# Kernel tuning notes

Hardware: AMD Instinct MI355X
Metric: run time of the kernel (lower is better)

Reference implementation:

```python
import jax, jax.numpy as jnp
import numpy as np

M = 12288   # anchor nodes
N = 12288   # neighbor nodes
D = 128     # out_features
TEMPERATURE = 0.07
NEG_PAD = jnp.float32(-2**32 + 1)  # same padding constant as torch code


def setup_inputs() -> dict:
    key = jax.random.key(0)
    k1, k2, k3, k4 = jax.random.split(key, 4)
    xx_anchor = jax.random.normal(k1, (M, D), dtype=jnp.float32)
    inp = jax.random.normal(k2, (N, D), dtype=jnp.float32)
    # sparse binary adjacency (~avg degree 25), stored dense int32 since the
    # module calls adj.to_dense() and only tests adj > 0
    adj = (jax.random.uniform(k3, (M, N)) < 0.002).astype(jnp.int32)
    # xavier_uniform-style init for the [D, D] attention weight
    limit = jnp.sqrt(6.0 / (D + D)).astype(jnp.float32)
    weight = jax.random.uniform(k4, (D, D), minval=-limit, maxval=limit, dtype=jnp.float32)
    return {"xx_anchor": xx_anchor, "input": inp, "adj": adj, "weight": weight}


def reference(xx_anchor, input, adj, weight):
    # scores[m, n] = (xx_anchor @ W) . input_n   -> dense [M, N]
    anchor_adj = jnp.einsum('md,de,ne->mn', xx_anchor, weight, input)
    scores = jnp.where(adj > 0, anchor_adj, NEG_PAD)
    atten = jax.nn.softmax(scores / TEMPERATURE, axis=1)  # row softmax over neighbors
    return atten @ input  # [M, D]
```

## Files before the change

### kernel.cpp

```cpp
#include <hip/hip_runtime.h>
#include <hip/hip_bf16.h>

#define M_ROWS 12288
#define N_COLS 12288
#define DDIM   128
#define MAXN   768
#define INV_T  (1.0f / 0.07f)

__global__ __launch_bounds__(256)
void layerconv_main(const float* __restrict__ xa,
                    const float* __restrict__ inp,
                    const int*   __restrict__ adj,
                    const float* __restrict__ wgt,
                    float*       __restrict__ out)
{
    const int m    = blockIdx.x;
    const int tid  = threadIdx.x;
    const int lane = tid & 63;
    const int wid  = tid >> 6;

    __shared__ float xarow[DDIM];
    __shared__ float ypart[2][DDIM];
    __shared__ float yrow[DDIM];
    __shared__ int   idx[MAXN];
    __shared__ float sc[MAXN];
    __shared__ int   cnt;
    __shared__ float inv_sum_s;

    if (tid == 0) cnt = 0;
    if (tid < DDIM) xarow[tid] = xa[(size_t)m * DDIM + tid];
    __syncthreads();

    {
        const int4* arow = (const int4*)(adj + (size_t)m * N_COLS);
        #pragma unroll
        for (int i = tid; i < N_COLS / 4; i += 256) {
            const int4 a = arow[i];
            if (a.x > 0) { int p = atomicAdd(&cnt, 1); if (p < MAXN) idx[p] = 4*i+0; }
            if (a.y > 0) { int p = atomicAdd(&cnt, 1); if (p < MAXN) idx[p] = 4*i+1; }
            if (a.z > 0) { int p = atomicAdd(&cnt, 1); if (p < MAXN) idx[p] = 4*i+2; }
            if (a.w > 0) { int p = atomicAdd(&cnt, 1); if (p < MAXN) idx[p] = 4*i+3; }
        }
    }

    {
        const int c  = tid & 127;
        const int kh = tid >> 7;
        float acc = 0.f;
        const float* wp = wgt + (size_t)(kh * 64) * DDIM + c;
        #pragma unroll 8
        for (int k = 0; k < 64; ++k)
            acc = fmaf(xarow[kh * 64 + k], wp[(size_t)k * DDIM], acc);
        ypart[kh][c] = acc;
    }
    __syncthreads();

    if (tid < DDIM) yrow[tid] = ypart[0][tid] + ypart[1][tid];
    const int cn = min(cnt, MAXN);
    __syncthreads();

    {
        const float y0 = yrow[2 * lane];
        const float y1 = yrow[2 * lane + 1];
        for (int j = wid; j < cn; j += 4) {
            const float2 v = ((const float2*)(inp + (size_t)idx[j] * DDIM))[lane];
            float s = fmaf(y0, v.x, y1 * v.y);
            #pragma unroll
            for (int off = 32; off > 0; off >>= 1) s += __shfl_down(s, off);
            if (lane == 0) sc[j] = s * INV_T;
        }
    }
    __syncthreads();

    if (tid == 0) {
        float mx = -INFINITY;
        for (int j = 0; j < cn; ++j) mx = fmaxf(mx, sc[j]);
        float sum = 0.f;
        for (int j = 0; j < cn; ++j) { float e = __expf(sc[j] - mx); sc[j] = e; sum += e; }
        inv_sum_s = 1.f / sum;
    }
    __syncthreads();

    if (tid < 64) {
        float a0 = 0.f, a1 = 0.f;
        if (cn > 0) {
            for (int j = 0; j < cn; ++j) {
                const float  w = sc[j];
                const float2 v = ((const float2*)(inp + (size_t)idx[j] * DDIM))[tid];
                a0 = fmaf(w, v.x, a0);
                a1 = fmaf(w, v.y, a1);
            }
            const float is = inv_sum_s;
            a0 *= is; a1 *= is;
        } else {
            for (int n = 0; n < N_COLS; ++n) {
                const float2 v = ((const float2*)(inp + (size_t)n * DDIM))[tid];
                a0 += v.x; a1 += v.y;
            }
            a0 /= (float)N_COLS; a1 /= (float)N_COLS;
        }
        ((float2*)(out + (size_t)m * DDIM))[tid] = make_float2(a0, a1);
    }
}

extern "C" void kernel_launch(void* const* d_in, const int* in_sizes, int n_in,
                              void* d_out, int out_size, void* d_ws, size_t ws_size,
                              hipStream_t stream) {
    const float* xa  = (const float*)d_in[0];
    const float* inp = (const float*)d_in[1];
    const int*   adj = (const int*)d_in[2];
    const float* wgt = (const float*)d_in[3];
    float* out = (float*)d_out;

    layerconv_main<<<M_ROWS, 256, 0, stream>>>(xa, inp, adj, wgt, out);
}
```

Before: 816.0 us.

## Map one wavefront per row with ballot compaction and online softmax

Each 64-lane wavefront now handles one anchor row independently, so a block covers four rows and all block barriers and shared atomics disappear. Neighbor indices are compacted with wavefront ballots and popcounts. The x·W projection is computed per wavefront using shuffles. The separate score, serial softmax and aggregation passes are fused into one online-softmax loop that reads each neighbor row once. The shared index buffer shrinks to 256 entries per row, which clamps rows of very high degree, and the single-row scan now runs on one wavefront instead of four.

```diff
diff --git a/kernel.cpp b/kernel.cpp
--- a/kernel.cpp
+++ b/kernel.cpp
@@ -4,103 +4,86 @@
 #define M_ROWS 12288
 #define N_COLS 12288
 #define DDIM   128
-#define MAXN   768
+#define MAXD   256
 #define INV_T  (1.0f / 0.07f)
 
-__global__ __launch_bounds__(256)
-void layerconv_main(const float* __restrict__ xa,
-                    const float* __restrict__ inp,
-                    const int*   __restrict__ adj,
-                    const float* __restrict__ wgt,
-                    float*       __restrict__ out)
+__global__ __launch_bounds__(256, 4)
+void layerconv_fused(const float* __restrict__ xa,
+                     const float* __restrict__ inp,
+                     const int*   __restrict__ adj,
+                     const float* __restrict__ wgt,
+                     float*       __restrict__ out)
 {
-    const int m    = blockIdx.x;
-    const int tid  = threadIdx.x;
-    const int lane = tid & 63;
-    const int wid  = tid >> 6;
+    __shared__ int idx[4][MAXD];
 
-    __shared__ float xarow[DDIM];
-    __shared__ float ypart[2][DDIM];
-    __shared__ float yrow[DDIM];
-    __shared__ int   idx[MAXN];
-    __shared__ float sc[MAXN];
-    __shared__ int   cnt;
-    __shared__ float inv_sum_s;
+    const int lane = threadIdx.x & 63;
+    const int wid  = threadIdx.x >> 6;
+    const int m    = blockIdx.x * 4 + wid;
 
-    if (tid == 0) cnt = 0;
-    if (tid < DDIM) xarow[tid] = xa[(size_t)m * DDIM + tid];
-    __syncthreads();
-
+    const float2 xv = ((const float2*)(xa + (size_t)m * DDIM))[lane];
+    float y0 = 0.f, y1 = 0.f;
     {
-        const int4* arow = (const int4*)(adj + (size_t)m * N_COLS);
-        #pragma unroll
-        for (int i = tid; i < N_COLS / 4; i += 256) {
-            const int4 a = arow[i];
-            if (a.x > 0) { int p = atomicAdd(&cnt, 1); if (p < MAXN) idx[p] = 4*i+0; }
-            if (a.y > 0) { int p = atomicAdd(&cnt, 1); if (p < MAXN) idx[p] = 4*i+1; }
-            if (a.z > 0) { int p = atomicAdd(&cnt, 1); if (p < MAXN) idx[p] = 4*i+2; }
-            if (a.w > 0) { int p = atomicAdd(&cnt, 1); if (p < MAXN) idx[p] = 4*i+3; }
+        const float2* wrow = (const float2*)wgt;
+        #pragma unroll 8
+        for (int k = 0; k < DDIM; ++k) {
+            const float  xak = __shfl((k & 1) ? xv.y : xv.x, k >> 1);
+            const float2 w   = wrow[(size_t)k * 64 + lane];
+            y0 = fmaf(xak, w.x, y0);
+            y1 = fmaf(xak, w.y, y1);
         }
     }
 
+    int cnt = 0;
     {
-        const int c  = tid & 127;
-        const int kh = tid >> 7;
-        float acc = 0.f;
-        const float* wp = wgt + (size_t)(kh * 64) * DDIM + c;
-        #pragma unroll 8
-        for (int k = 0; k < 64; ++k)
-            acc = fmaf(xarow[kh * 64 + k], wp[(size_t)k * DDIM], acc);
-        ypart[kh][c] = acc;
-    }
-    __syncthreads();
-
-    if (tid < DDIM) yrow[tid] = ypart[0][tid] + ypart[1][tid];
-    const int cn = min(cnt, MAXN);
-    __syncthreads();
-
-    {
-        const float y0 = yrow[2 * lane];
-        const float y1 = yrow[2 * lane + 1];
-        for (int j = wid; j < cn; j += 4) {
-            const float2 v = ((const float2*)(inp + (size_t)idx[j] * DDIM))[lane];
-            float s = fmaf(y0, v.x, y1 * v.y);
-            #pragma unroll
-            for (int off = 32; off > 0; off >>= 1) s += __shfl_down(s, off);
-            if (lane == 0) sc[j] = s * INV_T;
+        const int4* arow = (const int4*)(adj + (size_t)m * N_COLS);
+        const unsigned long long lt = (1ull << lane) - 1ull;
+        #pragma unroll 4
+        for (int i = lane; i < N_COLS / 4; i += 64) {
+            const int4 a = arow[i];
+            const unsigned long long b0 = __ballot(a.x > 0);
+            const unsigned long long b1 = __ballot(a.y > 0);
+            const unsigned long long b2 = __ballot(a.z > 0);
+            const unsigned long long b3 = __ballot(a.w > 0);
+            if (a.x > 0) idx[wid][min(cnt + (int)__popcll(b0 & lt), MAXD - 1)] = 4*i + 0;
+            cnt += (int)__popcll(b0);
+            if (a.y > 0) idx[wid][min(cnt + (int)__popcll(b1 & lt), MAXD - 1)] = 4*i + 1;
+            cnt += (int)__popcll(b1);
+            if (a.z > 0) idx[wid][min(cnt + (int)__popcll(b2 & lt), MAXD - 1)] = 4*i + 2;
+            cnt += (int)__popcll(b2);
+            if (a.w > 0) idx[wid][min(cnt + (int)__popcll(b3 & lt), MAXD - 1)] = 4*i + 3;
+            cnt += (int)__popcll(b3);
         }
     }
-    __syncthreads();
+    const int cn = min(cnt, MAXD);
 
-    if (tid == 0) {
-        float mx = -INFINITY;
-        for (int j = 0; j < cn; ++j) mx = fmaxf(mx, sc[j]);
-        float sum = 0.f;
-        for (int j = 0; j < cn; ++j) { float e = __expf(sc[j] - mx); sc[j] = e; sum += e; }
-        inv_sum_s = 1.f / sum;
+    float mrun = -INFINITY, lrun = 0.f, a0 = 0.f, a1 = 0.f;
+    for (int j = 0; j < cn; ++j) {
+        const int    n = idx[wid][j];
+        const float2 v = ((const float2*)(inp + (size_t)n * DDIM))[lane];
+        float s = fmaf(y0, v.x, y1 * v.y);
+        #pragma unroll
+        for (int off = 1; off < 64; off <<= 1) s += __shfl_xor(s, off);
+        s *= INV_T;
+        const float mnew  = fmaxf(mrun, s);
+        const float scale = __expf(mrun - mnew);
+        const float e     = __expf(s - mnew);
+        lrun = fmaf(lrun, scale, e);
+        a0   = fmaf(a0, scale, e * v.x);
+        a1   = fmaf(a1, scale, e * v.y);
+        mrun = mnew;
     }
-    __syncthreads();
 
-    if (tid < 64) {
-        float a0 = 0.f, a1 = 0.f;
-        if (cn > 0) {
-            for (int j = 0; j < cn; ++j) {
-                const float  w = sc[j];
-                const float2 v = ((const float2*)(inp + (size_t)idx[j] * DDIM))[tid];
-                a0 = fmaf(w, v.x, a0);
-                a1 = fmaf(w, v.y, a1);
-            }
-            const float is = inv_sum_s;
-            a0 *= is; a1 *= is;
-        } else {
-            for (int n = 0; n < N_COLS; ++n) {
-                const float2 v = ((const float2*)(inp + (size_t)n * DDIM))[tid];
-                a0 += v.x; a1 += v.y;
-            }
-            a0 /= (float)N_COLS; a1 /= (float)N_COLS;
+    if (cn > 0) {
+        const float inv = 1.f / lrun;
+        a0 *= inv; a1 *= inv;
+    } else {
+        for (int n = 0; n < N_COLS; ++n) {
+            const float2 v = ((const float2*)(inp + (size_t)n * DDIM))[lane];
+            a0 += v.x; a1 += v.y;
         }
-        ((float2*)(out + (size_t)m * DDIM))[tid] = make_float2(a0, a1);
+        a0 *= (1.f / N_COLS); a1 *= (1.f / N_COLS);
     }
+    ((float2*)(out + (size_t)m * DDIM))[lane] = make_float2(a0, a1);
 }
 
 extern "C" void kernel_launch(void* const* d_in, const int* in_sizes, int n_in,
@@ -112,5 +95,5 @@
     const float* wgt = (const float*)d_in[3];
     float* out = (float*)d_out;
 
-    layerconv_main<<<M_ROWS, 256, 0, stream>>>(xa, inp, adj, wgt, out);
+    layerconv_fused<<<M_ROWS / 4, 256, 0, stream>>>(xa, inp, adj, wgt, out);
 }
```

Measured after the change: 825.6 us. Within noise of the previous version (+1.2%).
